# Optimization experiments

Measured on AMD Instinct MI355X. Metric: run time of the kernel, lower is better.

Reference implementation:

```python
import jax, jax.numpy as jnp
import numpy as np

N = 100000   # nodes
E = 1600000  # edges
IN = 256
H = 128


def gcn_conv(x, W, b, src, dst, n):
    """PyG GCNConv (eval): self-loops + symmetric normalization + linear + scatter-add."""
    h = x @ W                                   # [n, out]
    loop = jnp.arange(n)
    s = jnp.concatenate([src, loop])            # [E+n]
    d = jnp.concatenate([dst, loop])
    deg = jax.ops.segment_sum(jnp.ones_like(d, dtype=h.dtype), d, num_segments=n)
    dinv = jnp.where(deg > 0, jax.lax.rsqrt(deg), 0.0)
    norm = dinv[s] * dinv[d]                    # [E+n]
    out = jax.ops.segment_sum(h[s] * norm[:, None], d, num_segments=n)
    return out + b


def setup_inputs() -> dict:
    key = jax.random.key(0)
    ks = jax.random.split(key, 8)
    x = jax.random.normal(ks[0], (N, IN), dtype=jnp.float32)
    edge_index = jax.random.randint(ks[1], (2, E), 0, N, dtype=jnp.int64)
    W1 = jax.random.normal(ks[2], (IN, H), dtype=jnp.float32) * (1.0 / np.sqrt(IN))
    b1 = jnp.zeros((H,), dtype=jnp.float32)
    W2 = jax.random.normal(ks[3], (H, H), dtype=jnp.float32) * (1.0 / np.sqrt(H))
    b2 = jnp.zeros((H,), dtype=jnp.float32)
    W3 = jax.random.normal(ks[4], (H, H), dtype=jnp.float32) * (1.0 / np.sqrt(H))
    b3 = jnp.zeros((H,), dtype=jnp.float32)
    return {"x": x, "edge_index": edge_index, "W1": W1, "b1": b1,
            "W2": W2, "b2": b2, "W3": W3, "b3": b3}


def reference(x, edge_index, W1, b1, W2, b2, W3, b3):
    src, dst = edge_index[0], edge_index[1]
    n = x.shape[0]
    h = gcn_conv(x, W1, b1, src, dst, n)
    h = jax.nn.relu(h)                          # dropout inactive in eval
    h = gcn_conv(h, W2, b2, src, dst, n)
    h = jax.nn.relu(h)
    h = gcn_conv(h, W3, b3, src, dst, n)
    return h
```

## Files before the change

kernel.cpp:

```cpp
#include <hip/hip_runtime.h>

#define HDIM 128

typedef unsigned int uint;
typedef unsigned short ushort;
typedef __attribute__((ext_vector_type(8))) short short8;
typedef __attribute__((ext_vector_type(4))) float f32x4;

__device__ inline ushort f2bf(float f) {
    uint u = __float_as_uint(f);
    uint rounding = 0x7fffu + ((u >> 16) & 1u);
    return (ushort)((u + rounding) >> 16);
}
__device__ inline float bf2f(ushort h) { return __uint_as_float(((uint)h) << 16); }

__device__ inline float4 bf4_to_f4(uint2 u) {
    float4 r;
    r.x = __uint_as_float(u.x << 16);
    r.y = __uint_as_float(u.x & 0xffff0000u);
    r.z = __uint_as_float(u.y << 16);
    r.w = __uint_as_float(u.y & 0xffff0000u);
    return r;
}


__global__ __launch_bounds__(256) void k_count(const int* __restrict__ dst,
                                               int* __restrict__ cnt,
                                               int* __restrict__ rank, int e) {
    int i = blockIdx.x * 256 + threadIdx.x;
    if (i < e) rank[i] = atomicAdd(&cnt[dst[i]], 1);
}

__global__ __launch_bounds__(256) void k_dinv(const int* __restrict__ cnt,
                                              float* __restrict__ dinv, int n) {
    int i = blockIdx.x * 256 + threadIdx.x;
    if (i < n) dinv[i] = rsqrtf((float)(cnt[i] + 1));
}

__global__ __launch_bounds__(256) void k_scan1(const int* __restrict__ cnt,
                                               int* __restrict__ offs,
                                               int* __restrict__ bsum, int n) {
    __shared__ int sm[256];
    int tid = threadIdx.x;
    int i = blockIdx.x * 256 + tid;
    int v = (i < n) ? cnt[i] : 0;
    sm[tid] = v;
    __syncthreads();
    for (int off = 1; off < 256; off <<= 1) {
        int t = (tid >= off) ? sm[tid - off] : 0;
        __syncthreads();
        sm[tid] += t;
        __syncthreads();
    }
    if (i < n) offs[i] = sm[tid] - v;
    if (tid == 255) bsum[blockIdx.x] = sm[255];
}

__global__ __launch_bounds__(512) void k_scan2(int* __restrict__ bsum, int nb) {
    __shared__ int sm[512];
    int tid = threadIdx.x;
    int v = (tid < nb) ? bsum[tid] : 0;
    sm[tid] = v;
    __syncthreads();
    for (int off = 1; off < 512; off <<= 1) {
        int t = (tid >= off) ? sm[tid - off] : 0;
        __syncthreads();
        sm[tid] += t;
        __syncthreads();
    }
    if (tid < nb) bsum[tid] = sm[tid] - v;
}

__global__ __launch_bounds__(256) void k_scan3(int* __restrict__ offs,
                                               const int* __restrict__ bsum,
                                               int n, int e) {
    int i = blockIdx.x * 256 + threadIdx.x;
    if (i < n) offs[i] += bsum[blockIdx.x];
    if (i == 0) offs[n] = e;
}

__global__ __launch_bounds__(256) void k_fill(const int* __restrict__ src,
                                              const int* __restrict__ dst,
                                              const int* __restrict__ offs,
                                              const int* __restrict__ rank,
                                              int* __restrict__ csr, int e) {
    int i = blockIdx.x * 256 + threadIdx.x;
    if (i < e) {
        csr[offs[dst[i]] + rank[i]] = src[i];
    }
}


__global__ __launch_bounds__(256) void k_prep_w(const float* __restrict__ W,
                                                ushort* __restrict__ wt_hi,
                                                ushort* __restrict__ wt_lo, int K) {
    int idx = blockIdx.x * 256 + threadIdx.x;
    if (idx < K * HDIM) {
        int k = idx >> 7;
        int c = idx & 127;
        float v = W[idx];
        ushort h = f2bf(v);
        ushort l = f2bf(v - bf2f(h));
        wt_hi[(size_t)c * K + k] = h;
        wt_lo[(size_t)c * K + k] = l;
    }
}


template<int K>
__global__ __launch_bounds__(256) void k_mm(const float* __restrict__ X,
                                            const ushort* __restrict__ wt_hi,
                                            const ushort* __restrict__ wt_lo,
                                            const float* __restrict__ dinv,
                                            ushort* __restrict__ g, int n)
{
    __shared__ ushort xh[128][40];
    __shared__ ushort xl[128][40];
    __shared__ ushort wh[128][40];
    __shared__ ushort wl[128][40];

    const int tid  = threadIdx.x;
    const int wv   = tid >> 6;
    const int lane = tid & 63;
    const int r    = lane & 15;
    const int gq   = lane >> 4;
    const int row0 = blockIdx.x * 128;

    const int srow  = tid >> 1;
    const int shalf = tid & 1;

    f32x4 acc[4][4];
    #pragma unroll
    for (int m = 0; m < 4; m++)
        #pragma unroll
        for (int nf = 0; nf < 4; nf++)
            acc[m][nf] = (f32x4){0.f, 0.f, 0.f, 0.f};

    const int xbase = (wv >> 1) * 64;
    const int wbase = (wv & 1) * 64;

    for (int k0 = 0; k0 < K; k0 += 32) {
        __syncthreads();
        {
            float4 f0, f1, f2, f3;
            int grow = row0 + srow;
            if (grow < n) {
                const float4* p = (const float4*)(X + (size_t)grow * K + k0 + shalf * 16);
                f0 = p[0]; f1 = p[1]; f2 = p[2]; f3 = p[3];
            } else {
                f0 = f1 = f2 = f3 = make_float4(0.f, 0.f, 0.f, 0.f);
            }
            float v[16] = {f0.x, f0.y, f0.z, f0.w, f1.x, f1.y, f1.z, f1.w,
                           f2.x, f2.y, f2.z, f2.w, f3.x, f3.y, f3.z, f3.w};
            uint h[8], l[8];
            #pragma unroll
            for (int q = 0; q < 8; q++) {
                ushort h0 = f2bf(v[2 * q]), h1 = f2bf(v[2 * q + 1]);
                h[q] = (uint)h0 | ((uint)h1 << 16);
                ushort l0 = f2bf(v[2 * q] - bf2f(h0));
                ushort l1 = f2bf(v[2 * q + 1] - bf2f(h1));
                l[q] = (uint)l0 | ((uint)l1 << 16);
            }
            *(uint4*)&xh[srow][shalf * 16]     = make_uint4(h[0], h[1], h[2], h[3]);
            *(uint4*)&xh[srow][shalf * 16 + 8] = make_uint4(h[4], h[5], h[6], h[7]);
            *(uint4*)&xl[srow][shalf * 16]     = make_uint4(l[0], l[1], l[2], l[3]);
            *(uint4*)&xl[srow][shalf * 16 + 8] = make_uint4(l[4], l[5], l[6], l[7]);
        }
        {
            const ushort* ph = wt_hi + (size_t)srow * K + k0 + shalf * 16;
            uint4 a0 = *(const uint4*)ph;
            uint4 a1 = *(const uint4*)(ph + 8);
            *(uint4*)&wh[srow][shalf * 16]     = a0;
            *(uint4*)&wh[srow][shalf * 16 + 8] = a1;
            const ushort* pl = wt_lo + (size_t)srow * K + k0 + shalf * 16;
            uint4 b0 = *(const uint4*)pl;
            uint4 b1 = *(const uint4*)(pl + 8);
            *(uint4*)&wl[srow][shalf * 16]     = b0;
            *(uint4*)&wl[srow][shalf * 16 + 8] = b1;
        }
        __syncthreads();

        short8 bh[4], bl[4];
        #pragma unroll
        for (int nf = 0; nf < 4; nf++) {
            bh[nf] = *(const short8*)&xh[xbase + nf * 16 + r][gq * 8];
            bl[nf] = *(const short8*)&xl[xbase + nf * 16 + r][gq * 8];
        }
        #pragma unroll
        for (int m = 0; m < 4; m++) {
            short8 ah = *(const short8*)&wh[wbase + m * 16 + r][gq * 8];
            short8 al = *(const short8*)&wl[wbase + m * 16 + r][gq * 8];
            #pragma unroll
            for (int nf = 0; nf < 4; nf++) {
                acc[m][nf] = __builtin_amdgcn_mfma_f32_16x16x32_bf16(ah, bh[nf], acc[m][nf], 0, 0, 0);
                acc[m][nf] = __builtin_amdgcn_mfma_f32_16x16x32_bf16(ah, bl[nf], acc[m][nf], 0, 0, 0);
                acc[m][nf] = __builtin_amdgcn_mfma_f32_16x16x32_bf16(al, bh[nf], acc[m][nf], 0, 0, 0);
            }
        }
    }

    #pragma unroll
    for (int nf = 0; nf < 4; nf++) {
        int xrow = row0 + xbase + nf * 16 + r;
        if (xrow < n) {
            float di = dinv[xrow];
            #pragma unroll
            for (int m = 0; m < 4; m++) {
                int wcol = wbase + m * 16 + gq * 4;
                f32x4 a = acc[m][nf];
                uint2 pk;
                pk.x = (uint)f2bf(a[0] * di) | ((uint)f2bf(a[1] * di) << 16);
                pk.y = (uint)f2bf(a[2] * di) | ((uint)f2bf(a[3] * di) << 16);
                *(uint2*)(g + (size_t)xrow * HDIM + wcol) = pk;
            }
        }
    }
}


template<bool RELU>
__global__ __launch_bounds__(256) void k_gather(const ushort* __restrict__ g,
                                                const int* __restrict__ csr,
                                                const int* __restrict__ offs,
                                                const float* __restrict__ dinv,
                                                const float* __restrict__ bias,
                                                float* __restrict__ out, int n)
{
    int t    = blockIdx.x * 256 + threadIdx.x;
    int node = t >> 5;
    int l    = t & 31;
    if (node >= n) return;

    int e0 = offs[node];
    int e1 = offs[node + 1];

    float4 acc = bf4_to_f4(*(const uint2*)(g + (size_t)node * HDIM + l * 4));

    int e = e0;
    for (; e + 4 <= e1; e += 4) {
        int s0 = csr[e], s1 = csr[e + 1], s2 = csr[e + 2], s3 = csr[e + 3];
        float4 v0 = bf4_to_f4(*(const uint2*)(g + (size_t)s0 * HDIM + l * 4));
        float4 v1 = bf4_to_f4(*(const uint2*)(g + (size_t)s1 * HDIM + l * 4));
        float4 v2 = bf4_to_f4(*(const uint2*)(g + (size_t)s2 * HDIM + l * 4));
        float4 v3 = bf4_to_f4(*(const uint2*)(g + (size_t)s3 * HDIM + l * 4));
        acc.x += v0.x + v1.x + v2.x + v3.x;
        acc.y += v0.y + v1.y + v2.y + v3.y;
        acc.z += v0.z + v1.z + v2.z + v3.z;
        acc.w += v0.w + v1.w + v2.w + v3.w;
    }
    for (; e < e1; e++) {
        int s = csr[e];
        float4 v = bf4_to_f4(*(const uint2*)(g + (size_t)s * HDIM + l * 4));
        acc.x += v.x; acc.y += v.y; acc.z += v.z; acc.w += v.w;
    }

    float di  = dinv[node];
    float4 bb = *(const float4*)(bias + l * 4);
    float4 o;
    o.x = fmaf(di, acc.x, bb.x);
    o.y = fmaf(di, acc.y, bb.y);
    o.z = fmaf(di, acc.z, bb.z);
    o.w = fmaf(di, acc.w, bb.w);
    if (RELU) {
        o.x = fmaxf(o.x, 0.f); o.y = fmaxf(o.y, 0.f);
        o.z = fmaxf(o.z, 0.f); o.w = fmaxf(o.w, 0.f);
    }
    *(float4*)(out + (size_t)node * HDIM + l * 4) = o;
}


extern "C" void kernel_launch(void* const* d_in, const int* in_sizes, int n_in,
                              void* d_out, int out_size, void* d_ws, size_t ws_size,
                              hipStream_t stream)
{
    const float* x  = (const float*)d_in[0];
    const int*   ei = (const int*)d_in[1];
    const float* W1 = (const float*)d_in[2];
    const float* b1 = (const float*)d_in[3];
    const float* W2 = (const float*)d_in[4];
    const float* b2 = (const float*)d_in[5];
    const float* W3 = (const float*)d_in[6];
    const float* b3 = (const float*)d_in[7];
    float* out = (float*)d_out;

    const int n = in_sizes[0] / 256;
    const int E = in_sizes[1] / 2;
    const int* src = ei;
    const int* dst = ei + E;

    char*   ws    = (char*)d_ws;
    float*  dinv  = (float*)(ws);
    int*    cnt   = (int*)(ws + (512 << 10));
    int*    offs  = (int*)(ws + (1 << 20));
    int*    bsum  = (int*)(ws + (1536 << 10));
    int*    csr   = (int*)(ws + (1600 << 10));
    int*    rank  = (int*)(ws + (8 << 20));
    ushort* wt_hi = (ushort*)(ws + (15 << 20));
    ushort* wt_lo = (ushort*)(ws + (15 << 20) + (128 << 10));
    ushort* g     = (ushort*)(ws + (16 << 20));

    dim3 blk(256);
    int ngrid = (n + 255) / 256;
    int egrid = (E + 255) / 256;

    hipMemsetAsync(cnt, 0, (size_t)n * 4, stream);
    k_count<<<egrid, blk, 0, stream>>>(dst, cnt, rank, E);
    k_dinv<<<ngrid, blk, 0, stream>>>(cnt, dinv, n);
    k_scan1<<<ngrid, blk, 0, stream>>>(cnt, offs, bsum, n);
    k_scan2<<<1, 512, 0, stream>>>(bsum, ngrid);
    k_scan3<<<ngrid, blk, 0, stream>>>(offs, bsum, n, E);
    k_fill<<<egrid, blk, 0, stream>>>(src, dst, offs, rank, csr, E);

    int mm_grid  = (n + 127) / 128;
    int gat_grid = (int)(((size_t)n * 32 + 255) / 256);

    k_prep_w<<<(256 * HDIM + 255) / 256, blk, 0, stream>>>(W1, wt_hi, wt_lo, 256);
    k_mm<256><<<mm_grid, blk, 0, stream>>>(x, wt_hi, wt_lo, dinv, g, n);
    k_gather<true><<<gat_grid, blk, 0, stream>>>(g, csr, offs, dinv, b1, out, n);
    k_prep_w<<<(128 * HDIM + 255) / 256, blk, 0, stream>>>(W2, wt_hi, wt_lo, 128);
    k_mm<128><<<mm_grid, blk, 0, stream>>>(out, wt_hi, wt_lo, dinv, g, n);
    k_gather<true><<<gat_grid, blk, 0, stream>>>(g, csr, offs, dinv, b2, out, n);
    k_prep_w<<<(128 * HDIM + 255) / 256, blk, 0, stream>>>(W3, wt_hi, wt_lo, 128);
    k_mm<128><<<mm_grid, blk, 0, stream>>>(out, wt_hi, wt_lo, dinv, g, n);
    k_gather<false><<<gat_grid, blk, 0, stream>>>(g, csr, offs, dinv, b3, out, n);
}
```

Measured before the change: 403.8 us.

## Emit bf16 hi/lo split from gather and load GEMM tiles via direct-to-LDS

The gather kernels for layers 1 and 2 now write the activation already split into bf16 hi and lo planes instead of fp32. The following GEMM then streams those planes, and the weight planes, straight into LDS with global_load_lds, dropping both the per-tile fp32-to-bf16 split and the register round trip. The LDS tiles lose their padding and now use a 32-wide unpadded layout, which may cause bank conflicts on the MFMA operand reads. A trailing barrier per k-step is added, and the out-of-range rows of the last tile are no longer zero-guarded in the direct-load path.

```diff
diff --git a/kernel.cpp b/kernel.cpp
--- a/kernel.cpp
+++ b/kernel.cpp
@@ -6,6 +6,10 @@
 typedef unsigned short ushort;
 typedef __attribute__((ext_vector_type(8))) short short8;
 typedef __attribute__((ext_vector_type(4))) float f32x4;
+
+typedef __attribute__((address_space(3))) uint  lds_u32_t;
+typedef const __attribute__((address_space(1))) uint g_u32_t;
+#define GLDS16(gp, lp) __builtin_amdgcn_global_load_lds((g_u32_t*)(gp), (lds_u32_t*)(lp), 16, 0, 0)
 
 __device__ inline ushort f2bf(float f) {
     uint u = __float_as_uint(f);
@@ -107,27 +111,34 @@
 }
 
 
-template<int K>
-__global__ __launch_bounds__(256) void k_mm(const float* __restrict__ X,
-                                            const ushort* __restrict__ wt_hi,
-                                            const ushort* __restrict__ wt_lo,
+template<int K, bool XF32>
+__global__ __launch_bounds__(256) void k_mm(const float* __restrict__ Xf,
+                                            const ushort* __restrict__ XH,
+                                            const ushort* __restrict__ XL,
+                                            const ushort* __restrict__ WH,
+                                            const ushort* __restrict__ WL,
                                             const float* __restrict__ dinv,
                                             ushort* __restrict__ g, int n)
 {
-    __shared__ ushort xh[128][40];
-    __shared__ ushort xl[128][40];
-    __shared__ ushort wh[128][40];
-    __shared__ ushort wl[128][40];
+    __shared__ ushort lds[4 * 4096];
 
     const int tid  = threadIdx.x;
     const int wv   = tid >> 6;
     const int lane = tid & 63;
     const int r    = lane & 15;
-    const int gq   = lane >> 4;
+    const int gq8  = (lane >> 4) * 8;
     const int row0 = blockIdx.x * 128;
 
-    const int srow  = tid >> 1;
-    const int shalf = tid & 1;
+    ushort* const Lxh = lds;
+    ushort* const Lxl = lds + 4096;
+    ushort* const Lwh = lds + 8192;
+    ushort* const Lwl = lds + 12288;
+
+    const ushort* plane = (wv == 0) ? XH : (wv == 1) ? XL : (wv == 2) ? WH : WL;
+    const size_t  rbase = (wv < 2) ? (size_t)row0 : 0;
+    ushort* const ldst  = lds + wv * 4096;
+    const int rsub = lane >> 2;
+    const int csub = (lane & 3) * 8;
 
     f32x4 acc[4][4];
     #pragma unroll
@@ -139,13 +150,22 @@
     const int xbase = (wv >> 1) * 64;
     const int wbase = (wv & 1) * 64;
 
+    const int srow  = tid >> 1;
+    const int shalf = tid & 1;
+
     for (int k0 = 0; k0 < K; k0 += 32) {
-        __syncthreads();
-        {
+        if constexpr (XF32) {
+            if (wv >= 2) {
+                #pragma unroll
+                for (int i = 0; i < 8; i++) {
+                    const ushort* gp = plane + (rbase + i * 16 + rsub) * (size_t)K + k0 + csub;
+                    GLDS16(gp, ldst + i * 512);
+                }
+            }
             float4 f0, f1, f2, f3;
             int grow = row0 + srow;
             if (grow < n) {
-                const float4* p = (const float4*)(X + (size_t)grow * K + k0 + shalf * 16);
+                const float4* p = (const float4*)(Xf + (size_t)grow * K + k0 + shalf * 16);
                 f0 = p[0]; f1 = p[1]; f2 = p[2]; f3 = p[3];
             } else {
                 f0 = f1 = f2 = f3 = make_float4(0.f, 0.f, 0.f, 0.f);
@@ -161,35 +181,30 @@
                 ushort l1 = f2bf(v[2 * q + 1] - bf2f(h1));
                 l[q] = (uint)l0 | ((uint)l1 << 16);
             }
-            *(uint4*)&xh[srow][shalf * 16]     = make_uint4(h[0], h[1], h[2], h[3]);
-            *(uint4*)&xh[srow][shalf * 16 + 8] = make_uint4(h[4], h[5], h[6], h[7]);
-            *(uint4*)&xl[srow][shalf * 16]     = make_uint4(l[0], l[1], l[2], l[3]);
-            *(uint4*)&xl[srow][shalf * 16 + 8] = make_uint4(l[4], l[5], l[6], l[7]);
-        }
-        {
-            const ushort* ph = wt_hi + (size_t)srow * K + k0 + shalf * 16;
-            uint4 a0 = *(const uint4*)ph;
-            uint4 a1 = *(const uint4*)(ph + 8);
-            *(uint4*)&wh[srow][shalf * 16]     = a0;
-            *(uint4*)&wh[srow][shalf * 16 + 8] = a1;
-            const ushort* pl = wt_lo + (size_t)srow * K + k0 + shalf * 16;
-            uint4 b0 = *(const uint4*)pl;
-            uint4 b1 = *(const uint4*)(pl + 8);
-            *(uint4*)&wl[srow][shalf * 16]     = b0;
-            *(uint4*)&wl[srow][shalf * 16 + 8] = b1;
+            int sb = srow * 32 + shalf * 16;
+            *(uint4*)&Lxh[sb]     = make_uint4(h[0], h[1], h[2], h[3]);
+            *(uint4*)&Lxh[sb + 8] = make_uint4(h[4], h[5], h[6], h[7]);
+            *(uint4*)&Lxl[sb]     = make_uint4(l[0], l[1], l[2], l[3]);
+            *(uint4*)&Lxl[sb + 8] = make_uint4(l[4], l[5], l[6], l[7]);
+        } else {
+            #pragma unroll
+            for (int i = 0; i < 8; i++) {
+                const ushort* gp = plane + (rbase + i * 16 + rsub) * (size_t)K + k0 + csub;
+                GLDS16(gp, ldst + i * 512);
+            }
         }
         __syncthreads();
 
         short8 bh[4], bl[4];
         #pragma unroll
         for (int nf = 0; nf < 4; nf++) {
-            bh[nf] = *(const short8*)&xh[xbase + nf * 16 + r][gq * 8];
-            bl[nf] = *(const short8*)&xl[xbase + nf * 16 + r][gq * 8];
+            bh[nf] = *(const short8*)&Lxh[(xbase + nf * 16 + r) * 32 + gq8];
+            bl[nf] = *(const short8*)&Lxl[(xbase + nf * 16 + r) * 32 + gq8];
         }
         #pragma unroll
         for (int m = 0; m < 4; m++) {
-            short8 ah = *(const short8*)&wh[wbase + m * 16 + r][gq * 8];
-            short8 al = *(const short8*)&wl[wbase + m * 16 + r][gq * 8];
+            short8 ah = *(const short8*)&Lwh[(wbase + m * 16 + r) * 32 + gq8];
+            short8 al = *(const short8*)&Lwl[(wbase + m * 16 + r) * 32 + gq8];
             #pragma unroll
             for (int nf = 0; nf < 4; nf++) {
                 acc[m][nf] = __builtin_amdgcn_mfma_f32_16x16x32_bf16(ah, bh[nf], acc[m][nf], 0, 0, 0);
@@ -197,6 +212,7 @@
                 acc[m][nf] = __builtin_amdgcn_mfma_f32_16x16x32_bf16(al, bh[nf], acc[m][nf], 0, 0, 0);
             }
         }
+        __syncthreads();
     }
 
     #pragma unroll
@@ -206,7 +222,7 @@
             float di = dinv[xrow];
             #pragma unroll
             for (int m = 0; m < 4; m++) {
-                int wcol = wbase + m * 16 + gq * 4;
+                int wcol = wbase + m * 16 + gq8 / 2;
                 f32x4 a = acc[m][nf];
                 uint2 pk;
                 pk.x = (uint)f2bf(a[0] * di) | ((uint)f2bf(a[1] * di) << 16);
@@ -218,13 +234,15 @@
 }
 
 
-template<bool RELU>
+template<bool RELU, bool EMIT_SPLIT>
 __global__ __launch_bounds__(256) void k_gather(const ushort* __restrict__ g,
                                                 const int* __restrict__ csr,
                                                 const int* __restrict__ offs,
                                                 const float* __restrict__ dinv,
                                                 const float* __restrict__ bias,
-                                                float* __restrict__ out, int n)
+                                                float* __restrict__ out,
+                                                ushort* __restrict__ ah,
+                                                ushort* __restrict__ al, int n)
 {
     int t    = blockIdx.x * 256 + threadIdx.x;
     int node = t >> 5;
@@ -265,7 +283,18 @@
         o.x = fmaxf(o.x, 0.f); o.y = fmaxf(o.y, 0.f);
         o.z = fmaxf(o.z, 0.f); o.w = fmaxf(o.w, 0.f);
     }
-    *(float4*)(out + (size_t)node * HDIM + l * 4) = o;
+    if (EMIT_SPLIT) {
+        ushort h0 = f2bf(o.x), h1 = f2bf(o.y), h2 = f2bf(o.z), h3 = f2bf(o.w);
+        uint2 ph, pl;
+        ph.x = (uint)h0 | ((uint)h1 << 16);
+        ph.y = (uint)h2 | ((uint)h3 << 16);
+        pl.x = (uint)f2bf(o.x - bf2f(h0)) | ((uint)f2bf(o.y - bf2f(h1)) << 16);
+        pl.y = (uint)f2bf(o.z - bf2f(h2)) | ((uint)f2bf(o.w - bf2f(h3)) << 16);
+        *(uint2*)(ah + (size_t)node * HDIM + l * 4) = ph;
+        *(uint2*)(al + (size_t)node * HDIM + l * 4) = pl;
+    } else {
+        *(float4*)(out + (size_t)node * HDIM + l * 4) = o;
+    }
 }
 
 
@@ -288,16 +317,18 @@
     const int* src = ei;
     const int* dst = ei + E;
 
-    char*   ws    = (char*)d_ws;
-    float*  dinv  = (float*)(ws);
-    int*    cnt   = (int*)(ws + (512 << 10));
-    int*    offs  = (int*)(ws + (1 << 20));
-    int*    bsum  = (int*)(ws + (1536 << 10));
-    int*    csr   = (int*)(ws + (1600 << 10));
-    int*    rank  = (int*)(ws + (8 << 20));
-    ushort* wt_hi = (ushort*)(ws + (15 << 20));
-    ushort* wt_lo = (ushort*)(ws + (15 << 20) + (128 << 10));
-    ushort* g     = (ushort*)(ws + (16 << 20));
+    char*   ws   = (char*)d_ws;
+    float*  dinv = (float*)(ws);
+    int*    cnt  = (int*)(ws + (512 << 10));
+    int*    offs = (int*)(ws + (1 << 20));
+    int*    bsum = (int*)(ws + 1536 * 1024);
+    int*    csr  = (int*)(ws + 1600 * 1024);
+    int*    rank = (int*)(ws + (size_t)(8 << 20));
+    ushort* wh   = (ushort*)(ws + 14848 * 1024);
+    ushort* wl   = (ushort*)(ws + 15104 * 1024);
+    ushort* g    = (ushort*)(ws + (size_t)(16 << 20));
+    ushort* xh2  = (ushort*)(ws + (size_t)(42 << 20));
+    ushort* xl2  = (ushort*)(ws + (size_t)(68 << 20));
 
     dim3 blk(256);
     int ngrid = (n + 255) / 256;
@@ -314,13 +345,13 @@
     int mm_grid  = (n + 127) / 128;
     int gat_grid = (int)(((size_t)n * 32 + 255) / 256);
 
-    k_prep_w<<<(256 * HDIM + 255) / 256, blk, 0, stream>>>(W1, wt_hi, wt_lo, 256);
-    k_mm<256><<<mm_grid, blk, 0, stream>>>(x, wt_hi, wt_lo, dinv, g, n);
-    k_gather<true><<<gat_grid, blk, 0, stream>>>(g, csr, offs, dinv, b1, out, n);
-    k_prep_w<<<(128 * HDIM + 255) / 256, blk, 0, stream>>>(W2, wt_hi, wt_lo, 128);
-    k_mm<128><<<mm_grid, blk, 0, stream>>>(out, wt_hi, wt_lo, dinv, g, n);
-    k_gather<true><<<gat_grid, blk, 0, stream>>>(g, csr, offs, dinv, b2, out, n);
-    k_prep_w<<<(128 * HDIM + 255) / 256, blk, 0, stream>>>(W3, wt_hi, wt_lo, 128);
-    k_mm<128><<<mm_grid, blk, 0, stream>>>(out, wt_hi, wt_lo, dinv, g, n);
-    k_gather<false><<<gat_grid, blk, 0, stream>>>(g, csr, offs, dinv, b3, out, n);
-}
+    k_prep_w<<<(256 * HDIM + 255) / 256, blk, 0, stream>>>(W1, wh, wl, 256);
+    k_mm<256, true><<<mm_grid, blk, 0, stream>>>(x, nullptr, nullptr, wh, wl, dinv, g, n);
+    k_gather<true, true><<<gat_grid, blk, 0, stream>>>(g, csr, offs, dinv, b1, nullptr, xh2, xl2, n);
+    k_prep_w<<<(128 * HDIM + 255) / 256, blk, 0, stream>>>(W2, wh, wl, 128);
+    k_mm<128, false><<<mm_grid, blk, 0, stream>>>(nullptr, xh2, xl2, wh, wl, dinv, g, n);
+    k_gather<true, true><<<gat_grid, blk, 0, stream>>>(g, csr, offs, dinv, b2, nullptr, xh2, xl2, n);
+    k_prep_w<<<(128 * HDIM + 255) / 256, blk, 0, stream>>>(W3, wh, wl, 128);
+    k_mm<128, false><<<mm_grid, blk, 0, stream>>>(nullptr, xh2, xl2, wh, wl, dinv, g, n);
+    k_gather<false, false><<<gat_grid, blk, 0, stream>>>(g, csr, offs, dinv, b3, out, nullptr, nullptr, n);
+}
```

New measurement: 405.9 us. Within noise of the previous version (+0.5%).
